# Optimization experiments

Hardware: AMD Instinct MI355X
Metric: run time of the kernel (lower is better)

Reference implementation:

```python
import jax, jax.numpy as jnp
import numpy as np

N_NODES = 10000
N_EDGES = 320000
D_IN = 256
D_HID = 256
N_CLASSES = 40


def _init_linear(key, fan_in, fan_out):
    kw, kb = jax.random.split(key)
    bound = 1.0 / np.sqrt(fan_in)
    W = jax.random.uniform(kw, (fan_in, fan_out), jnp.float32, -bound, bound)
    b = jax.random.uniform(kb, (fan_out,), jnp.float32, -bound, bound)
    return W, b


def setup_inputs() -> dict:
    key = jax.random.key(0)
    k0, k1, k2, k3, k4 = jax.random.split(key, 5)
    node_features = jax.random.normal(k0, (N_NODES, D_IN), jnp.float32)
    edge_index = jax.random.randint(k1, (2, N_EDGES), 0, N_NODES, jnp.int64)
    W1, b1 = _init_linear(k2, D_IN, D_HID)
    W2, b2 = _init_linear(k3, D_HID, D_HID)
    W3, b3 = _init_linear(k4, D_HID, N_CLASSES)
    return {"node_features": node_features, "edge_index": edge_index,
            "W1": W1, "b1": b1, "W2": W2, "b2": b2, "W3": W3, "b3": b3}


def _mp_layer(x, src, dst, W, b):
    # message: linear transform of source-node features (transform-then-gather
    # is mathematically identical to gather-then-transform and cheaper when E>N)
    msg = (x @ W + b)[src]                      # [E, d_out]
    # scatter sum-aggregate messages at destination nodes
    out = jax.ops.segment_sum(msg, dst, num_segments=N_NODES)  # [N, d_out]
    return out


def reference(node_features, edge_index, W1, b1, W2, b2, W3, b3):
    src, dst = edge_index[0], edge_index[1]
    x = jax.nn.relu(_mp_layer(node_features, src, dst, W1, b1))
    x = jax.nn.relu(_mp_layer(x, src, dst, W2, b2))
    x = jax.nn.relu(_mp_layer(x, src, dst, W3, b3))
    return x
```

## Files before the change

kernel.cpp:

```cpp
#include <hip/hip_runtime.h>


#define N_NODES   10000
#define N_EDGES   320000
#define D_HID     256
#define N_CLASSES 40
#define CAP       96

typedef __attribute__((ext_vector_type(8))) short short8;
typedef __attribute__((ext_vector_type(4))) float f32x4;

__device__ __forceinline__ ushort f2bf(float f) {
    unsigned u = __float_as_uint(f);
    u = (u + 0x7fffu + ((u >> 16) & 1u)) >> 16;
    return (ushort)u;
}
__device__ __forceinline__ float bf2f(ushort u) {
    return __uint_as_float(((unsigned)u) << 16);
}


__global__ __launch_bounds__(256)
void prep_kernel(const float* __restrict__ X,
                 const float* __restrict__ W1, const float* __restrict__ W2,
                 const float* __restrict__ W3,
                 ushort* __restrict__ Xb, ushort* __restrict__ bufY,
                 ushort* __restrict__ bufH,
                 ushort* __restrict__ W1b, ushort* __restrict__ W2b,
                 ushort* __restrict__ W3b, int* __restrict__ cursor) {
    __shared__ float tile[64][65];
    const int tid = threadIdx.x;
    if (blockIdx.x < 32) {
        const float* W  = (blockIdx.x < 16) ? W1 : W2;
        ushort* Wb      = (blockIdx.x < 16) ? W1b : W2b;
        const int b  = blockIdx.x & 15;
        const int k0 = (b >> 2) * 64, n0 = (b & 3) * 64;
        const int lane64 = tid & 63, quad = tid >> 6;
#pragma unroll
        for (int i = 0; i < 16; ++i) {
            int kl = quad + i * 4;
            tile[lane64][kl] = W[(size_t)(k0 + kl) * 256 + n0 + lane64];
        }
        __syncthreads();
#pragma unroll
        for (int i = 0; i < 16; ++i) {
            int nl = quad + i * 4;
            Wb[(size_t)(n0 + nl) * 256 + k0 + lane64] = f2bf(tile[nl][lane64]);
        }
        return;
    }
    const int tid0 = (blockIdx.x - 32) * 256 + tid;
    const int nthr = (gridDim.x - 32) * 256;
    for (int i = tid0; i < N_NODES; i += nthr) cursor[i] = 0;
    ushort4 z; z.x = 0; z.y = 0; z.z = 0; z.w = 0;
    if (tid0 < 64) {
        ((ushort4*)Xb)[640000 + tid0]   = z;
        ((ushort4*)bufY)[640000 + tid0] = z;
    }
    if (tid0 < 10) ((ushort4*)bufH)[100000 + tid0] = z;
    for (int i = tid0; i < N_NODES * D_HID / 4; i += nthr) {
        float4 v = ((const float4*)X)[i];
        ushort4 o;
        o.x = f2bf(v.x); o.y = f2bf(v.y); o.z = f2bf(v.z); o.w = f2bf(v.w);
        ((ushort4*)Xb)[i] = o;
    }
    for (int i = tid0; i < N_CLASSES * 256; i += nthr) {
        int n = i >> 8, k = i & 255;
        W3b[i] = f2bf(W3[(size_t)k * N_CLASSES + n]);
    }
}


__global__ __launch_bounds__(256)
void place_kernel(const int* __restrict__ edges, int* __restrict__ cursor,
                  int* __restrict__ esrc) {
    int e = blockIdx.x * 256 + threadIdx.x;
    if (e < N_EDGES) {
        int d = edges[N_EDGES + e];
        int pos = atomicAdd(&cursor[d], 1);
        if (pos < CAP) esrc[d * CAP + pos] = edges[e];
    }
}


#define LDSA 264
#define LDSB 44

template<bool CHAIN>
__global__ __launch_bounds__(256)
void layer_kernel(const ushort* __restrict__ Xin, const ushort* __restrict__ Bt,
                  const float* __restrict__ bias,
                  const int* __restrict__ deg, const int* __restrict__ esrc,
                  const ushort* __restrict__ W3b, const float* __restrict__ b3,
                  ushort* __restrict__ Out) {
    __shared__ ushort As[16 * LDSA];
    __shared__ ushort Bs[256 * LDSB];
    __shared__ int    eidxL[16 * CAP];
    __shared__ int    degI[16];
    __shared__ float  degF[16];

    const int tid = threadIdx.x;
    const int wave = tid >> 6, lane = tid & 63;
    const int lr = lane & 15, lg = lane >> 4;
    const int rowBase = blockIdx.x * 16;

#pragma unroll
    for (int p = 0; p < 6; ++p) {
        int idx = p * 256 + tid;
        eidxL[idx] = esrc[rowBase * CAP + idx];
    }
    if (tid < 16) {
        int c = deg[rowBase + tid];
        degF[tid] = (float)c;
        degI[tid] = (c > CAP) ? CAP : c;
    }
    __syncthreads();

    const uint2* hp = (const uint2*)Xin;
#pragma unroll 1
    for (int it = 0; it < 4; ++it) {
        int nl = wave * 4 + it;
        const int cnt  = degI[nl];
        const int cntp = (cnt + 7) & ~7;
        float a0 = 0.f, a1 = 0.f, a2 = 0.f, a3 = 0.f;
#pragma unroll 1
        for (int i = 0; i < cntp; i += 8) {
            uint2 v[8];
#pragma unroll
            for (int u = 0; u < 8; ++u) {
                int slot = i + u;
                int s = (slot < cnt) ? eidxL[nl * CAP + slot] : N_NODES;
                v[u] = hp[(size_t)s * 64 + lane];
            }
#pragma unroll
            for (int u = 0; u < 8; ++u) {
                a0 += bf2f((ushort)(v[u].x & 0xffff));
                a1 += bf2f((ushort)(v[u].x >> 16));
                a2 += bf2f((ushort)(v[u].y & 0xffff));
                a3 += bf2f((ushort)(v[u].y >> 16));
            }
        }
        uint2 o;
        o.x = (unsigned)f2bf(a0) | ((unsigned)f2bf(a1) << 16);
        o.y = (unsigned)f2bf(a2) | ((unsigned)f2bf(a3) << 16);
        *(uint2*)(As + nl * LDSA + lane * 4) = o;
    }

    f32x4 acc[4] = {};
    for (int k0 = 0; k0 < 256; k0 += 32) {
        __syncthreads();
#pragma unroll
        for (int p = 0; p < 4; ++p) {
            int idx = p * 256 + tid;
            int n = idx >> 2, c = (idx & 3) * 8;
            *(uint4*)(Bs + n * LDSB + c) = *(const uint4*)(Bt + (size_t)n * 256 + k0 + c);
        }
        __syncthreads();
        short8 af = *(const short8*)(As + lr * LDSA + k0 + lg * 8);
#pragma unroll
        for (int j = 0; j < 4; ++j) {
            short8 bf = *(const short8*)(Bs + (wave * 64 + j * 16 + lr) * LDSB + lg * 8);
            acc[j] = __builtin_amdgcn_mfma_f32_16x16x32_bf16(af, bf, acc[j], 0, 0, 0);
        }
    }

    if (!CHAIN) {
#pragma unroll
        for (int j = 0; j < 4; ++j) {
            int col = wave * 64 + j * 16 + lr;
            float bv = bias[col];
#pragma unroll
            for (int r = 0; r < 4; ++r) {
                int grow = rowBase + lg * 4 + r;
                float dg = degF[lg * 4 + r];
                Out[(size_t)grow * 256 + col] = f2bf(fmaxf(fmaf(dg, bv, acc[j][r]), 0.f));
            }
        }
    } else {
        __syncthreads();
#pragma unroll
        for (int j = 0; j < 4; ++j) {
            int col = wave * 64 + j * 16 + lr;
            float bv = bias[col];
#pragma unroll
            for (int r = 0; r < 4; ++r) {
                int rl = lg * 4 + r;
                As[rl * LDSA + col] = f2bf(fmaxf(fmaf(degF[rl], bv, acc[j][r]), 0.f));
            }
        }
#pragma unroll
        for (int p = 0; p < 5; ++p) {
            int idx = p * 256 + tid;
            int n = idx >> 5, c = (idx & 31) * 8;
            *(uint4*)(Bs + n * LDSA + c) = *(const uint4*)(W3b + (size_t)n * 256 + c);
        }
        __syncthreads();
        if (wave < 3) {
            f32x4 acc3 = {};
            for (int k0 = 0; k0 < 256; k0 += 32) {
                short8 af = *(const short8*)(As + lr * LDSA + k0 + lg * 8);
                short8 bf = *(const short8*)(Bs + (wave * 16 + lr) * LDSA + k0 + lg * 8);
                acc3 = __builtin_amdgcn_mfma_f32_16x16x32_bf16(af, bf, acc3, 0, 0, 0);
            }
            int col = wave * 16 + lr;
            if (col < N_CLASSES) {
                float bv = b3[col];
#pragma unroll
                for (int r = 0; r < 4; ++r) {
                    int grow = rowBase + lg * 4 + r;
                    Out[(size_t)grow * N_CLASSES + col] = f2bf(acc3[r] + bv);
                }
            }
        }
    }
}


__global__ __launch_bounds__(256)
void agg_relu_40_kernel(const ushort* __restrict__ h, const int* __restrict__ deg,
                        const int* __restrict__ esrc, float* __restrict__ out) {
    int wv   = threadIdx.x >> 6;
    int lane = threadIdx.x & 63;
    int node = (blockIdx.x << 2) + wv;
    if (node >= N_NODES) return;
    int cnt = deg[node];
    if (cnt > CAP) cnt = CAP;
    int cntp = (cnt + 7) & ~7;
    const int* ep = esrc + node * CAP;
    if (lane < N_CLASSES) {
        float a = 0.f, b = 0.f;
#pragma unroll 1
        for (int i = 0; i < cntp; i += 8) {
            int s[8];
#pragma unroll
            for (int u = 0; u < 8; ++u) s[u] = (i + u < cnt) ? ep[i + u] : N_NODES;
#pragma unroll
            for (int u = 0; u < 8; u += 2) {
                a += bf2f(h[(size_t)s[u]     * N_CLASSES + lane]);
                b += bf2f(h[(size_t)s[u + 1] * N_CLASSES + lane]);
            }
        }
        out[(size_t)node * N_CLASSES + lane] = fmaxf(a + b, 0.f);
    }
}


extern "C" void kernel_launch(void* const* d_in, const int* in_sizes, int n_in,
                              void* d_out, int out_size, void* d_ws, size_t ws_size,
                              hipStream_t stream) {
    const float* X     = (const float*)d_in[0];
    const int*   edges = (const int*)d_in[1];
    const float* W1 = (const float*)d_in[2];
    const float* b1 = (const float*)d_in[3];
    const float* W2 = (const float*)d_in[4];
    const float* b2 = (const float*)d_in[5];
    const float* W3 = (const float*)d_in[6];
    const float* b3 = (const float*)d_in[7];
    float* out = (float*)d_out;

    char* ws = (char*)d_ws;
    ushort* Xb   = (ushort*)(ws);
    ushort* bufY = (ushort*)(ws + 5120512);
    ushort* bufH = (ushort*)(ws + 10241024);
    ushort* W1b  = (ushort*)(ws + 11041104);
    ushort* W2b  = (ushort*)(ws + 11172176);
    ushort* W3b  = (ushort*)(ws + 11303248);
    int*   cursor = (int*)(ws + 11323728);
    int*   esrc   = (int*)(ws + 11363728);

    prep_kernel<<<288, 256, 0, stream>>>(X, W1, W2, W3, Xb, bufY, bufH,
                                         W1b, W2b, W3b, cursor);
    place_kernel<<<(N_EDGES + 255) / 256, 256, 0, stream>>>(edges, cursor, esrc);
    layer_kernel<false><<<N_NODES / 16, 256, 0, stream>>>(
        Xb, W1b, b1, cursor, esrc, W3b, b3, bufY);
    layer_kernel<true><<<N_NODES / 16, 256, 0, stream>>>(
        bufY, W2b, b2, cursor, esrc, W3b, b3, bufH);
    agg_relu_40_kernel<<<(N_NODES + 3) / 4, 256, 0, stream>>>(bufH, cursor, esrc, out);
}
```

Measured before the change: 173.9 us.

## Pre-fill edge slots with sentinel and split gather into two 128-column halves

The edge-slot table is pre-filled with the dummy zero-row index in the prep kernel, so the aggregation loops drop their per-slot bounds check and read indices directly. The layer kernel's neighbor gather now runs in two passes over 128-column halves with 4-byte loads instead of one pass with 8-byte loads. This is meant to shrink the per-pass row footprint for better cache locality and remove the select logic. In exchange it adds a full 960K-int fill in prep and runs the index loop twice.

```diff
diff --git a/kernel.cpp b/kernel.cpp
--- a/kernel.cpp
+++ b/kernel.cpp
@@ -27,7 +27,8 @@
                  ushort* __restrict__ Xb, ushort* __restrict__ bufY,
                  ushort* __restrict__ bufH,
                  ushort* __restrict__ W1b, ushort* __restrict__ W2b,
-                 ushort* __restrict__ W3b, int* __restrict__ cursor) {
+                 ushort* __restrict__ W3b, int* __restrict__ cursor,
+                 int* __restrict__ esrc) {
     __shared__ float tile[64][65];
     const int tid = threadIdx.x;
     if (blockIdx.x < 32) {
@@ -52,6 +53,7 @@
     const int tid0 = (blockIdx.x - 32) * 256 + tid;
     const int nthr = (gridDim.x - 32) * 256;
     for (int i = tid0; i < N_NODES; i += nthr) cursor[i] = 0;
+    for (int i = tid0; i < N_NODES * CAP; i += nthr) esrc[i] = N_NODES;
     ushort4 z; z.x = 0; z.y = 0; z.z = 0; z.w = 0;
     if (tid0 < 64) {
         ((ushort4*)Xb)[640000 + tid0]   = z;
@@ -116,34 +118,31 @@
     }
     __syncthreads();
 
-    const uint2* hp = (const uint2*)Xin;
-#pragma unroll 1
-    for (int it = 0; it < 4; ++it) {
-        int nl = wave * 4 + it;
-        const int cnt  = degI[nl];
-        const int cntp = (cnt + 7) & ~7;
-        float a0 = 0.f, a1 = 0.f, a2 = 0.f, a3 = 0.f;
-#pragma unroll 1
-        for (int i = 0; i < cntp; i += 8) {
-            uint2 v[8];
-#pragma unroll
-            for (int u = 0; u < 8; ++u) {
-                int slot = i + u;
-                int s = (slot < cnt) ? eidxL[nl * CAP + slot] : N_NODES;
-                v[u] = hp[(size_t)s * 64 + lane];
-            }
-#pragma unroll
-            for (int u = 0; u < 8; ++u) {
-                a0 += bf2f((ushort)(v[u].x & 0xffff));
-                a1 += bf2f((ushort)(v[u].x >> 16));
-                a2 += bf2f((ushort)(v[u].y & 0xffff));
-                a3 += bf2f((ushort)(v[u].y >> 16));
-            }
-        }
-        uint2 o;
-        o.x = (unsigned)f2bf(a0) | ((unsigned)f2bf(a1) << 16);
-        o.y = (unsigned)f2bf(a2) | ((unsigned)f2bf(a3) << 16);
-        *(uint2*)(As + nl * LDSA + lane * 4) = o;
+    const uint* hp = (const uint*)Xin;
+#pragma unroll 1
+    for (int half = 0; half < 2; ++half) {
+#pragma unroll 1
+        for (int it = 0; it < 4; ++it) {
+            int nl = wave * 4 + it;
+            const int cntp = (degI[nl] + 7) & ~7;
+            float a0 = 0.f, a1 = 0.f;
+#pragma unroll 1
+            for (int i = 0; i < cntp; i += 8) {
+                uint v[8];
+#pragma unroll
+                for (int u = 0; u < 8; ++u) {
+                    int s = eidxL[nl * CAP + i + u];
+                    v[u] = hp[(size_t)s * 128 + half * 64 + lane];
+                }
+#pragma unroll
+                for (int u = 0; u < 8; ++u) {
+                    a0 += bf2f((ushort)(v[u] & 0xffff));
+                    a1 += bf2f((ushort)(v[u] >> 16));
+                }
+            }
+            unsigned o = (unsigned)f2bf(a0) | ((unsigned)f2bf(a1) << 16);
+            *(unsigned*)(As + nl * LDSA + half * 128 + lane * 2) = o;
+        }
     }
 
     f32x4 acc[4] = {};
@@ -233,7 +232,7 @@
         for (int i = 0; i < cntp; i += 8) {
             int s[8];
 #pragma unroll
-            for (int u = 0; u < 8; ++u) s[u] = (i + u < cnt) ? ep[i + u] : N_NODES;
+            for (int u = 0; u < 8; ++u) s[u] = ep[i + u];
 #pragma unroll
             for (int u = 0; u < 8; u += 2) {
                 a += bf2f(h[(size_t)s[u]     * N_CLASSES + lane]);
@@ -269,7 +268,7 @@
     int*   esrc   = (int*)(ws + 11363728);
 
     prep_kernel<<<288, 256, 0, stream>>>(X, W1, W2, W3, Xb, bufY, bufH,
-                                         W1b, W2b, W3b, cursor);
+                                         W1b, W2b, W3b, cursor, esrc);
     place_kernel<<<(N_EDGES + 255) / 256, 256, 0, stream>>>(edges, cursor, esrc);
     layer_kernel<false><<<N_NODES / 16, 256, 0, stream>>>(
         Xb, W1b, b1, cursor, esrc, W3b, b3, bufY);
```

After: 170.5 us. -2.0%, faster.
